# Kernel optimization log

Measured on AMD Instinct MI355X. Metric: run time of the kernel, lower is better.

## Reference

```python
import jax, jax.numpy as jnp
import numpy as np

T, B, D, NQ = 2048, 256, 128, 4  # time, batch, input_dim, n_qubits(=hidden_dim)
H = NQ


def setup_inputs() -> dict:
    key = jax.random.key(0)
    ks = jax.random.split(key, 13)
    inp = {"inputs": jax.random.normal(ks[0], (T, B, D), dtype=jnp.float32)}
    s = 1.0 / np.sqrt(D + H)  # nn.Linear default init bound
    for idx, name in enumerate(["forget", "input", "update", "output"]):
        kw, kb, kt = jax.random.split(ks[1 + idx], 3)
        inp[f"W_{name}"] = jax.random.uniform(kw, (D + H, NQ), jnp.float32, -s, s)
        inp[f"b_{name}"] = jax.random.uniform(kb, (NQ,), jnp.float32, -s, s)
        # trainable RX angles of the quantum gate layer
        inp[f"theta_{name}"] = jax.random.uniform(kt, (NQ,), jnp.float32, 0.0, 2.0 * np.pi)
    return inp


def _qlayer(x, theta):
    """Analytic simulation of the QLayer circuit.

    Circuit: RX(x_i) then RX(theta_i) on wire i (== RX(x_i+theta_i) on |0>),
    then CNOT chain (0->1, 1->2, ...), then <Z_k> on every wire.
    Heisenberg picture: Z_k pulled back through the CNOT chain becomes
    Z_0 Z_1 ... Z_k, and on the product state <Z_i> = cos(x_i + theta_i),
    so the measurement on wire k is the cumulative product of cosines.
    """
    return jnp.cumprod(jnp.cos(x + theta), axis=-1)


def reference(inputs, W_forget, b_forget, theta_forget,
              W_input, b_input, theta_input,
              W_update, b_update, theta_update,
              W_output, b_output, theta_output):
    bsz = inputs.shape[1]
    hd = theta_forget.shape[0]  # hidden_dim == n_qubits
    h0 = jnp.zeros((bsz, hd), inputs.dtype)
    c0 = jnp.zeros((bsz, hd), inputs.dtype)

    def step(carry, x):
        hx, cx = carry
        comb = jnp.concatenate([x, hx], axis=1)          # [B, D+H]
        f = jax.nn.sigmoid(_qlayer(comb @ W_forget + b_forget, theta_forget))
        i = jax.nn.sigmoid(_qlayer(comb @ W_input + b_input, theta_input))
        g = jnp.tanh(_qlayer(comb @ W_update + b_update, theta_update))
        o = jax.nn.sigmoid(_qlayer(comb @ W_output + b_output, theta_output))
        cx = f * cx + i * g
        hx = o * jnp.tanh(cx)
        return (hx, cx), hx

    (hx, cx), outputs = jax.lax.scan(step, (h0, c0), inputs)
    return outputs, hx, cx
```

## Files before the change

kernel.cpp:

```cpp
#include <hip/hip_runtime.h>
#include <hip/hip_bf16.h>

#define T_STEPS 2048
#define BATCH   256
#define DIM     128
#define INV2PI  0.15915494309189535f

#define ZX_FLOATS (T_STEPS * BATCH * 16)

__global__ __launch_bounds__(64) void prep(
    const float* __restrict__ Wf, const float* __restrict__ bf, const float* __restrict__ tf,
    const float* __restrict__ Wi, const float* __restrict__ bi, const float* __restrict__ ti,
    const float* __restrict__ Wu, const float* __restrict__ bu, const float* __restrict__ tu,
    const float* __restrict__ Wo, const float* __restrict__ bo, const float* __restrict__ to_,
    float* __restrict__ Wc, float* __restrict__ bt)
{
    const int tid = threadIdx.x;
    for (int idx = tid; idx < DIM * 16; idx += 64) {
        int d = idx >> 4, u = idx & 15, g = u >> 2, k = u & 3;
        const float* W = (g == 0) ? Wf : (g == 1) ? Wi : (g == 2) ? Wu : Wo;
        Wc[idx] = W[d * 4 + k] * INV2PI;
    }
    if (tid < 16) {
        int g = tid >> 2, k = tid & 3;
        const float* bb = (g == 0) ? bf : (g == 1) ? bi : (g == 2) ? bo : bo;
        const float* tt = (g == 0) ? tf : (g == 1) ? ti : (g == 2) ? tu : to_;
        const float* btab[4] = { bf, bi, bu, bo };
        const float* ttab[4] = { tf, ti, tu, to_ };
        bb = btab[g]; tt = ttab[g];
        bt[tid] = (bb[k] + tt[k]) * INV2PI;
    }
}

__global__ __launch_bounds__(256) void zx_gemm(
    const float4* __restrict__ x4,
    const float*  __restrict__ Wc,
    const float*  __restrict__ btv,
    float4*       __restrict__ Zx4)
{
    __shared__ float xs[4][64 * 36];
    const int lane = threadIdx.x & 63;
    const int wid  = threadIdx.x >> 6;
    float* myxs = xs[wid];
    const size_t wrow0 = ((size_t)blockIdx.x * 4 + wid) * 64;

    float acc[16];
#pragma unroll
    for (int u = 0; u < 16; ++u) acc[u] = btv[u];

    const int r0 = lane >> 3;
    const int q  = lane & 7;

#pragma unroll
    for (int c = 0; c < 4; ++c) {
        float4 v[8];
#pragma unroll
        for (int i = 0; i < 8; ++i)
            v[i] = x4[(wrow0 + i * 8 + r0) * 32 + c * 8 + q];
#pragma unroll
        for (int i = 0; i < 8; ++i)
            *(float4*)&myxs[(i * 8 + r0) * 36 + q * 4] = v[i];

        float xr[32];
#pragma unroll
        for (int j = 0; j < 8; ++j) {
            float4 tv = *(const float4*)&myxs[lane * 36 + j * 4];
            xr[j * 4 + 0] = tv.x; xr[j * 4 + 1] = tv.y;
            xr[j * 4 + 2] = tv.z; xr[j * 4 + 3] = tv.w;
        }
#pragma unroll
        for (int dd = 0; dd < 32; ++dd) {
            const float xv = xr[dd];
            const float* w = &Wc[(c * 32 + dd) * 16];
#pragma unroll
            for (int u = 0; u < 16; ++u) acc[u] = fmaf(xv, w[u], acc[u]);
        }
    }

    size_t orow = wrow0 + lane;
    float4* zr = &Zx4[orow * 4];
    zr[0] = make_float4(acc[0],  acc[1],  acc[2],  acc[3]);
    zr[1] = make_float4(acc[4],  acc[5],  acc[6],  acc[7]);
    zr[2] = make_float4(acc[8],  acc[9],  acc[10], acc[11]);
    zr[3] = make_float4(acc[12], acc[13], acc[14], acc[15]);
}

template<int CTRL>
__device__ __forceinline__ float fdpp(float x) {
    return __int_as_float(__builtin_amdgcn_update_dpp(
        0, __float_as_int(x), CTRL, 0xF, 0xF, true));
}

__device__ __forceinline__ float lstm_step(
    float& h, float& c, float zb,
    float wh0, float wh1, float wh2, float wh3,
    float s1c, float m2, float m3, int k, bool b0g, bool b1g)
{
    float h0 = fdpp<0x00>(h), h1 = fdpp<0x55>(h), h2 = fdpp<0xAA>(h), h3 = fdpp<0xFF>(h);
    float t1 = fmaf(h2, wh2, h3 * wh3);
    float z  = fmaf(h1, wh1, fmaf(h0, wh0, zb)) + t1;

    float cs = __builtin_amdgcn_cosf(__builtin_amdgcn_fractf(z));

    float q0 = fdpp<0x00>(cs), q1 = fdpp<0x55>(cs), q2 = fdpp<0xAA>(cs);
    float p = (q0 * (k >= 1 ? q1 : 1.f)) * ((k >= 2 ? q2 : 1.f) * (k == 3 ? cs : 1.f));

    float e = __builtin_amdgcn_exp2f(p * s1c);
    float y = fmaf(__builtin_amdgcn_rcpf(1.f + e), m2, m3);

    float mm  = fdpp<0x1B>(y);
    float y4  = fdpp<0x141>(mm);
    float y8  = fdpp<0x128>(y);
    float y12 = fdpp<0x128>(y4);
    float t01  = b0g ? y4  : y,  t01s = b0g ? y  : y4;
    float t23  = b0g ? y12 : y8, t23s = b0g ? y8 : y12;
    float fv = b1g ? t23  : t01;
    float iv = b1g ? t23s : t01s;
    float gv = b1g ? t01  : t23;
    float ov = b1g ? t01s : t23s;

    c = fmaf(fv, c, iv * gv);
    float e2 = __builtin_amdgcn_exp2f(c * -2.885390082f);
    float th = fmaf(2.f, __builtin_amdgcn_rcpf(1.f + e2), -1.f);
    h = ov * th;
    return h;
}

__global__ __launch_bounds__(64) void qlstm_rec(
    const float* __restrict__ Zx,
    const float* __restrict__ Wf, const float* __restrict__ Wi,
    const float* __restrict__ Wu, const float* __restrict__ Wo,
    float* __restrict__ out)
{
    const int tid = threadIdx.x;
    const int u   = tid & 15;
    const int g   = u >> 2;
    const int k   = u & 3;
    const int b   = blockIdx.x * 4 + (tid >> 4);

    const float* Wg = (g == 0) ? Wf : (g == 1) ? Wi : (g == 2) ? Wu : Wo;
    const float wh0 = Wg[(DIM + 0) * 4 + k] * INV2PI;
    const float wh1 = Wg[(DIM + 1) * 4 + k] * INV2PI;
    const float wh2 = Wg[(DIM + 2) * 4 + k] * INV2PI;
    const float wh3 = Wg[(DIM + 3) * 4 + k] * INV2PI;

    const bool  isg = (g == 2);
    const float s1c = isg ? -2.885390082f : -1.442695041f;
    const float m2  = isg ? 2.f : 1.f;
    const float m3  = isg ? -1.f : 0.f;
    const bool  b0g = (g & 1) != 0;
    const bool  b1g = (g & 2) != 0;

    const float* zp = Zx + b * 16 + u;
    const bool do_store = (u < 4);
    float* op = out + b * 4 + k;

    float h = 0.f, c = 0.f;

    float zv[8];
#pragma unroll
    for (int i = 0; i < 8; ++i) zv[i] = zp[(size_t)i * 4096];

    for (int t = 0; t < T_STEPS; t += 8) {
#pragma unroll
        for (int j = 0; j < 8; ++j) {
            int tt = t + j;

            float o = lstm_step(h, c, zv[j], wh0, wh1, wh2, wh3, s1c, m2, m3, k, b0g, b1g);

            if (do_store) op[(size_t)tt * (BATCH * 4)] = o;

            int tn = tt + 8;
            if (tn > T_STEPS - 1) tn = T_STEPS - 1;
            zv[j] = zp[(size_t)tn * 4096];
        }
    }

    if (do_store) {
        size_t hx_off = (size_t)T_STEPS * BATCH * 4;
        out[hx_off + b * 4 + k] = h;
        out[hx_off + BATCH * 4 + b * 4 + k] = c;
    }
}

extern "C" void kernel_launch(void* const* d_in, const int* in_sizes, int n_in,
                              void* d_out, int out_size, void* d_ws, size_t ws_size,
                              hipStream_t stream) {
    const float* x  = (const float*)d_in[0];
    const float* Wf = (const float*)d_in[1];
    const float* bf = (const float*)d_in[2];
    const float* tf = (const float*)d_in[3];
    const float* Wi = (const float*)d_in[4];
    const float* bi = (const float*)d_in[5];
    const float* ti = (const float*)d_in[6];
    const float* Wu = (const float*)d_in[7];
    const float* bu = (const float*)d_in[8];
    const float* tu = (const float*)d_in[9];
    const float* Wo = (const float*)d_in[10];
    const float* bo = (const float*)d_in[11];
    const float* to_ = (const float*)d_in[12];
    float* out = (float*)d_out;

    float* Zx = (float*)d_ws;
    float* Wc = Zx + ZX_FLOATS;
    float* bt = Wc + DIM * 16;

    prep<<<1, 64, 0, stream>>>(Wf, bf, tf, Wi, bi, ti, Wu, bu, tu, Wo, bo, to_, Wc, bt);

    zx_gemm<<<(T_STEPS * BATCH) / 256, 256, 0, stream>>>(
        (const float4*)x, Wc, bt, (float4*)Zx);

    qlstm_rec<<<BATCH / 4, 64, 0, stream>>>(Zx, Wf, Wi, Wu, Wo, out);
}
```

Before: 676.7 us.

## Fuse input projection GEMM into recurrent LSTM kernel with double-buffered LDS staging

```diff
diff --git a/kernel.cpp b/kernel.cpp
--- a/kernel.cpp
+++ b/kernel.cpp
@@ -5,8 +5,6 @@
 #define BATCH   256
 #define DIM     128
 #define INV2PI  0.15915494309189535f
-
-#define ZX_FLOATS (T_STEPS * BATCH * 16)
 
 __global__ __launch_bounds__(64) void prep(
     const float* __restrict__ Wf, const float* __restrict__ bf, const float* __restrict__ tf,
@@ -23,66 +21,10 @@
     }
     if (tid < 16) {
         int g = tid >> 2, k = tid & 3;
-        const float* bb = (g == 0) ? bf : (g == 1) ? bi : (g == 2) ? bo : bo;
+        const float* bb = (g == 0) ? bf : (g == 1) ? bi : (g == 2) ? bu : bo;
         const float* tt = (g == 0) ? tf : (g == 1) ? ti : (g == 2) ? tu : to_;
-        const float* btab[4] = { bf, bi, bu, bo };
-        const float* ttab[4] = { tf, ti, tu, to_ };
-        bb = btab[g]; tt = ttab[g];
         bt[tid] = (bb[k] + tt[k]) * INV2PI;
     }
-}
-
-__global__ __launch_bounds__(256) void zx_gemm(
-    const float4* __restrict__ x4,
-    const float*  __restrict__ Wc,
-    const float*  __restrict__ btv,
-    float4*       __restrict__ Zx4)
-{
-    __shared__ float xs[4][64 * 36];
-    const int lane = threadIdx.x & 63;
-    const int wid  = threadIdx.x >> 6;
-    float* myxs = xs[wid];
-    const size_t wrow0 = ((size_t)blockIdx.x * 4 + wid) * 64;
-
-    float acc[16];
-#pragma unroll
-    for (int u = 0; u < 16; ++u) acc[u] = btv[u];
-
-    const int r0 = lane >> 3;
-    const int q  = lane & 7;
-
-#pragma unroll
-    for (int c = 0; c < 4; ++c) {
-        float4 v[8];
-#pragma unroll
-        for (int i = 0; i < 8; ++i)
-            v[i] = x4[(wrow0 + i * 8 + r0) * 32 + c * 8 + q];
-#pragma unroll
-        for (int i = 0; i < 8; ++i)
-            *(float4*)&myxs[(i * 8 + r0) * 36 + q * 4] = v[i];
-
-        float xr[32];
-#pragma unroll
-        for (int j = 0; j < 8; ++j) {
-            float4 tv = *(const float4*)&myxs[lane * 36 + j * 4];
-            xr[j * 4 + 0] = tv.x; xr[j * 4 + 1] = tv.y;
-            xr[j * 4 + 2] = tv.z; xr[j * 4 + 3] = tv.w;
-        }
-#pragma unroll
-        for (int dd = 0; dd < 32; ++dd) {
-            const float xv = xr[dd];
-            const float* w = &Wc[(c * 32 + dd) * 16];
-#pragma unroll
-            for (int u = 0; u < 16; ++u) acc[u] = fmaf(xv, w[u], acc[u]);
-        }
-    }
-
-    size_t orow = wrow0 + lane;
-    float4* zr = &Zx4[orow * 4];
-    zr[0] = make_float4(acc[0],  acc[1],  acc[2],  acc[3]);
-    zr[1] = make_float4(acc[4],  acc[5],  acc[6],  acc[7]);
-    zr[2] = make_float4(acc[8],  acc[9],  acc[10], acc[11]);
-    zr[3] = make_float4(acc[12], acc[13], acc[14], acc[15]);
 }
 
 template<int CTRL>
@@ -126,17 +68,27 @@
     return h;
 }
 
-__global__ __launch_bounds__(64) void qlstm_rec(
-    const float* __restrict__ Zx,
+__global__ __launch_bounds__(64) void qlstm_fused(
+    const float4* __restrict__ x4,
+    const float*  __restrict__ Wc,
+    const float*  __restrict__ btv,
     const float* __restrict__ Wf, const float* __restrict__ Wi,
     const float* __restrict__ Wu, const float* __restrict__ Wo,
     float* __restrict__ out)
 {
+    __shared__ float xbuf[2][32 * 144];
+
     const int tid = threadIdx.x;
+    const int q   = tid >> 4;
     const int u   = tid & 15;
     const int g   = u >> 2;
     const int k   = u & 3;
-    const int b   = blockIdx.x * 4 + (tid >> 4);
+    const int b   = blockIdx.x;
+
+    float wq[32];
+#pragma unroll
+    for (int dd = 0; dd < 32; ++dd) wq[dd] = Wc[(q * 32 + dd) * 16 + u];
+    const float btu = btv[u];
 
     const float* Wg = (g == 0) ? Wf : (g == 1) ? Wi : (g == 2) ? Wu : Wo;
     const float wh0 = Wg[(DIM + 0) * 4 + k] * INV2PI;
@@ -151,29 +103,79 @@
     const bool  b0g = (g & 1) != 0;
     const bool  b1g = (g & 2) != 0;
 
-    const float* zp = Zx + b * 16 + u;
-    const bool do_store = (u < 4);
+    const bool do_store = (tid < 4);
     float* op = out + b * 4 + k;
 
     float h = 0.f, c = 0.f;
-
-    float zv[8];
-#pragma unroll
-    for (int i = 0; i < 8; ++i) zv[i] = zp[(size_t)i * 4096];
-
-    for (int t = 0; t < T_STEPS; t += 8) {
-#pragma unroll
-        for (int j = 0; j < 8; ++j) {
-            int tt = t + j;
-
-            float o = lstm_step(h, c, zv[j], wh0, wh1, wh2, wh3, s1c, m2, m3, k, b0g, b1g);
-
-            if (do_store) op[(size_t)tt * (BATCH * 4)] = o;
-
-            int tn = tt + 8;
-            if (tn > T_STEPS - 1) tn = T_STEPS - 1;
-            zv[j] = zp[(size_t)tn * 4096];
-        }
+    int pb = 0;
+
+    float4 sx[16];
+
+    auto stage_load = [&](int w) {
+        const int t0 = w * 32;
+#pragma unroll
+        for (int m = 0; m < 16; ++m) {
+            int G = m * 64 + tid, s = G >> 5, cc = G & 31;
+            sx[m] = x4[((size_t)(t0 + s) * BATCH + b) * 32 + cc];
+        }
+    };
+    auto stage_write = [&](int dst) {
+#pragma unroll
+        for (int m = 0; m < 16; ++m) {
+            int G = m * 64 + tid, s = G >> 5, cc = G & 31;
+            *(float4*)&xbuf[dst][s * 144 + (cc >> 3) * 36 + (cc & 7) * 4] = sx[m];
+        }
+    };
+    auto zx_full = [&](int slot, int buf) -> float {
+        const float* xp = &xbuf[buf][slot * 144 + q * 36];
+        float a0 = 0.f, a1 = 0.f;
+#pragma unroll
+        for (int j = 0; j < 8; j += 2) {
+            float4 xa = *(const float4*)&xp[j * 4];
+            float4 xb = *(const float4*)&xp[j * 4 + 4];
+            a0 = fmaf(xa.x, wq[4 * j + 0], a0);
+            a0 = fmaf(xa.y, wq[4 * j + 1], a0);
+            a0 = fmaf(xa.z, wq[4 * j + 2], a0);
+            a0 = fmaf(xa.w, wq[4 * j + 3], a0);
+            a1 = fmaf(xb.x, wq[4 * j + 4], a1);
+            a1 = fmaf(xb.y, wq[4 * j + 5], a1);
+            a1 = fmaf(xb.z, wq[4 * j + 6], a1);
+            a1 = fmaf(xb.w, wq[4 * j + 7], a1);
+        }
+        float v = a0 + a1;
+        v += __shfl_xor(v, 32);
+        v += __shfl_xor(v, 16);
+        return v + btu;
+    };
+
+    stage_load(0);
+    stage_write(0);
+    float zxc = zx_full(0, 0);
+
+    for (int w = 0; w < 64; ++w) {
+        if (w < 63) stage_load(w + 1);
+#pragma unroll 4
+        for (int s = 0; s < 16; ++s) {
+            float zxn = zx_full(s + 1, pb);
+            float o = lstm_step(h, c, zxc, wh0, wh1, wh2, wh3, s1c, m2, m3, k, b0g, b1g);
+            if (do_store) op[(size_t)(w * 32 + s) * (BATCH * 4)] = o;
+            zxc = zxn;
+        }
+        if (w < 63) stage_write(pb ^ 1);
+#pragma unroll 3
+        for (int s = 16; s < 31; ++s) {
+            float zxn = zx_full(s + 1, pb);
+            float o = lstm_step(h, c, zxc, wh0, wh1, wh2, wh3, s1c, m2, m3, k, b0g, b1g);
+            if (do_store) op[(size_t)(w * 32 + s) * (BATCH * 4)] = o;
+            zxc = zxn;
+        }
+        {
+            float zxn = zx_full(0, pb ^ 1);
+            float o = lstm_step(h, c, zxc, wh0, wh1, wh2, wh3, s1c, m2, m3, k, b0g, b1g);
+            if (do_store) op[(size_t)(w * 32 + 31) * (BATCH * 4)] = o;
+            zxc = zxn;
+        }
+        pb ^= 1;
     }
 
     if (do_store) {
@@ -201,14 +203,11 @@
     const float* to_ = (const float*)d_in[12];
     float* out = (float*)d_out;
 
-    float* Zx = (float*)d_ws;
-    float* Wc = Zx + ZX_FLOATS;
+    float* Wc = (float*)d_ws;
     float* bt = Wc + DIM * 16;
 
     prep<<<1, 64, 0, stream>>>(Wf, bf, tf, Wi, bi, ti, Wu, bu, tu, Wo, bo, to_, Wc, bt);
 
-    zx_gemm<<<(T_STEPS * BATCH) / 256, 256, 0, stream>>>(
-        (const float4*)x, Wc, bt, (float4*)Zx);
-
-    qlstm_rec<<<BATCH / 4, 64, 0, stream>>>(Zx, Wf, Wi, Wu, Wo, out);
-}
+    qlstm_fused<<<BATCH, 64, 0, stream>>>(
+        (const float4*)x, Wc, bt, Wf, Wi, Wu, Wo, out);
+}
```

After: 937.2 us. 38.5% more time.

## Restructure input projection GEMM with register-resident weights and pipelined staging

Applied to the files above, without the earlier changes.

```diff
diff --git a/kernel.cpp b/kernel.cpp
--- a/kernel.cpp
+++ b/kernel.cpp
@@ -23,11 +23,8 @@
     }
     if (tid < 16) {
         int g = tid >> 2, k = tid & 3;
-        const float* bb = (g == 0) ? bf : (g == 1) ? bi : (g == 2) ? bo : bo;
+        const float* bb = (g == 0) ? bf : (g == 1) ? bi : (g == 2) ? bu : bo;
         const float* tt = (g == 0) ? tf : (g == 1) ? ti : (g == 2) ? tu : to_;
-        const float* btab[4] = { bf, bi, bu, bo };
-        const float* ttab[4] = { tf, ti, tu, to_ };
-        bb = btab[g]; tt = ttab[g];
         bt[tid] = (bb[k] + tt[k]) * INV2PI;
     }
 }
@@ -36,53 +33,79 @@
     const float4* __restrict__ x4,
     const float*  __restrict__ Wc,
     const float*  __restrict__ btv,
-    float4*       __restrict__ Zx4)
-{
-    __shared__ float xs[4][64 * 36];
+    float*        __restrict__ Zx)
+{
+    __shared__ float xs[4][16 * 144];
     const int lane = threadIdx.x & 63;
     const int wid  = threadIdx.x >> 6;
     float* myxs = xs[wid];
-    const size_t wrow0 = ((size_t)blockIdx.x * 4 + wid) * 64;
-
-    float acc[16];
-#pragma unroll
-    for (int u = 0; u < 16; ++u) acc[u] = btv[u];
-
-    const int r0 = lane >> 3;
-    const int q  = lane & 7;
-
-#pragma unroll
-    for (int c = 0; c < 4; ++c) {
-        float4 v[8];
-#pragma unroll
-        for (int i = 0; i < 8; ++i)
-            v[i] = x4[(wrow0 + i * 8 + r0) * 32 + c * 8 + q];
-#pragma unroll
-        for (int i = 0; i < 8; ++i)
-            *(float4*)&myxs[(i * 8 + r0) * 36 + q * 4] = v[i];
-
-        float xr[32];
-#pragma unroll
-        for (int j = 0; j < 8; ++j) {
-            float4 tv = *(const float4*)&myxs[lane * 36 + j * 4];
-            xr[j * 4 + 0] = tv.x; xr[j * 4 + 1] = tv.y;
-            xr[j * 4 + 2] = tv.z; xr[j * 4 + 3] = tv.w;
-        }
-#pragma unroll
-        for (int dd = 0; dd < 32; ++dd) {
-            const float xv = xr[dd];
-            const float* w = &Wc[(c * 32 + dd) * 16];
-#pragma unroll
-            for (int u = 0; u < 16; ++u) acc[u] = fmaf(xv, w[u], acc[u]);
-        }
-    }
-
-    size_t orow = wrow0 + lane;
-    float4* zr = &Zx4[orow * 4];
-    zr[0] = make_float4(acc[0],  acc[1],  acc[2],  acc[3]);
-    zr[1] = make_float4(acc[4],  acc[5],  acc[6],  acc[7]);
-    zr[2] = make_float4(acc[8],  acc[9],  acc[10], acc[11]);
-    zr[3] = make_float4(acc[12], acc[13], acc[14], acc[15]);
+
+    const int q = lane >> 4;
+    const int u = lane & 15;
+
+    float wq[32];
+#pragma unroll
+    for (int dd = 0; dd < 32; ++dd) wq[dd] = Wc[(q * 32 + dd) * 16 + u];
+    const float btu = btv[u];
+
+    const size_t WR0 = ((size_t)blockIdx.x * 4 + wid) * 128;
+
+    float4 sx[8];
+    auto stage_load = [&](size_t r0) {
+#pragma unroll
+        for (int m = 0; m < 8; ++m) {
+            int G = m * 64 + lane, s = G >> 5, cc = G & 31;
+            sx[m] = x4[(r0 + s) * 32 + cc];
+        }
+    };
+    auto stage_write = [&]() {
+#pragma unroll
+        for (int m = 0; m < 8; ++m) {
+            int G = m * 64 + lane, s = G >> 5, cc = G & 31;
+            *(float4*)&myxs[s * 144 + (cc >> 3) * 36 + (cc & 7) * 4] = sx[m];
+        }
+    };
+    auto zx_row = [&](int r) -> float {
+        const float* xp = &myxs[r * 144 + q * 36];
+        float a0 = 0.f, a1 = 0.f;
+#pragma unroll
+        for (int j = 0; j < 8; j += 2) {
+            float4 xa = *(const float4*)&xp[j * 4];
+            float4 xb = *(const float4*)&xp[j * 4 + 4];
+            a0 = fmaf(xa.x, wq[4 * j + 0], a0);
+            a0 = fmaf(xa.y, wq[4 * j + 1], a0);
+            a0 = fmaf(xa.z, wq[4 * j + 2], a0);
+            a0 = fmaf(xa.w, wq[4 * j + 3], a0);
+            a1 = fmaf(xb.x, wq[4 * j + 4], a1);
+            a1 = fmaf(xb.y, wq[4 * j + 5], a1);
+            a1 = fmaf(xb.z, wq[4 * j + 6], a1);
+            a1 = fmaf(xb.w, wq[4 * j + 7], a1);
+        }
+        float v = a0 + a1;
+        v += __shfl_xor(v, 32);
+        v += __shfl_xor(v, 16);
+        return v + btu;
+    };
+
+    stage_load(WR0);
+    stage_write();
+
+    for (int i = 0; i < 8; ++i) {
+        const size_t r0 = WR0 + (size_t)i * 16;
+        if (i < 7) stage_load(r0 + 16);
+
+#pragma unroll
+        for (int rr = 0; rr < 16; rr += 4) {
+            float z0 = zx_row(rr + 0);
+            float z1 = zx_row(rr + 1);
+            float z2 = zx_row(rr + 2);
+            float z3 = zx_row(rr + 3);
+            float vout = (q == 0) ? z0 : (q == 1) ? z1 : (q == 2) ? z2 : z3;
+            Zx[(r0 + rr + q) * 16 + u] = vout;
+        }
+
+        if (i < 7) stage_write();
+    }
 }
 
 template<int CTRL>
@@ -207,8 +230,8 @@
 
     prep<<<1, 64, 0, stream>>>(Wf, bf, tf, Wi, bi, ti, Wu, bu, tu, Wo, bo, to_, Wc, bt);
 
-    zx_gemm<<<(T_STEPS * BATCH) / 256, 256, 0, stream>>>(
-        (const float4*)x, Wc, bt, (float4*)Zx);
+    zx_gemm<<<(T_STEPS * BATCH) / 512, 256, 0, stream>>>(
+        (const float4*)x, Wc, bt, Zx);
 
     qlstm_rec<<<BATCH / 4, 64, 0, stream>>>(Zx, Wf, Wi, Wu, Wo, out);
 }
```

Result: slower. 721.7 us (+6.7%).

## Merge input GEMM and recurrence into one kernel with windowed flag sync

Applied to the files above, without the earlier changes.

```diff
diff --git a/kernel.cpp b/kernel.cpp
--- a/kernel.cpp
+++ b/kernel.cpp
@@ -7,13 +7,17 @@
 #define INV2PI  0.15915494309189535f
 
 #define ZX_FLOATS (T_STEPS * BATCH * 16)
+#define NTILES   8192
+#define NWIN     64
+#define TPW      128
+#define NGEMMW   960
 
 __global__ __launch_bounds__(64) void prep(
     const float* __restrict__ Wf, const float* __restrict__ bf, const float* __restrict__ tf,
     const float* __restrict__ Wi, const float* __restrict__ bi, const float* __restrict__ ti,
     const float* __restrict__ Wu, const float* __restrict__ bu, const float* __restrict__ tu,
     const float* __restrict__ Wo, const float* __restrict__ bo, const float* __restrict__ to_,
-    float* __restrict__ Wc, float* __restrict__ bt)
+    float* __restrict__ Wc, float* __restrict__ bt, unsigned int* __restrict__ wcnt)
 {
     const int tid = threadIdx.x;
     for (int idx = tid; idx < DIM * 16; idx += 64) {
@@ -23,66 +27,11 @@
     }
     if (tid < 16) {
         int g = tid >> 2, k = tid & 3;
-        const float* bb = (g == 0) ? bf : (g == 1) ? bi : (g == 2) ? bo : bo;
+        const float* bb = (g == 0) ? bf : (g == 1) ? bi : (g == 2) ? bu : bo;
         const float* tt = (g == 0) ? tf : (g == 1) ? ti : (g == 2) ? tu : to_;
-        const float* btab[4] = { bf, bi, bu, bo };
-        const float* ttab[4] = { tf, ti, tu, to_ };
-        bb = btab[g]; tt = ttab[g];
         bt[tid] = (bb[k] + tt[k]) * INV2PI;
     }
-}
-
-__global__ __launch_bounds__(256) void zx_gemm(
-    const float4* __restrict__ x4,
-    const float*  __restrict__ Wc,
-    const float*  __restrict__ btv,
-    float4*       __restrict__ Zx4)
-{
-    __shared__ float xs[4][64 * 36];
-    const int lane = threadIdx.x & 63;
-    const int wid  = threadIdx.x >> 6;
-    float* myxs = xs[wid];
-    const size_t wrow0 = ((size_t)blockIdx.x * 4 + wid) * 64;
-
-    float acc[16];
-#pragma unroll
-    for (int u = 0; u < 16; ++u) acc[u] = btv[u];
-
-    const int r0 = lane >> 3;
-    const int q  = lane & 7;
-
-#pragma unroll
-    for (int c = 0; c < 4; ++c) {
-        float4 v[8];
-#pragma unroll
-        for (int i = 0; i < 8; ++i)
-            v[i] = x4[(wrow0 + i * 8 + r0) * 32 + c * 8 + q];
-#pragma unroll
-        for (int i = 0; i < 8; ++i)
-            *(float4*)&myxs[(i * 8 + r0) * 36 + q * 4] = v[i];
-
-        float xr[32];
-#pragma unroll
-        for (int j = 0; j < 8; ++j) {
-            float4 tv = *(const float4*)&myxs[lane * 36 + j * 4];
-            xr[j * 4 + 0] = tv.x; xr[j * 4 + 1] = tv.y;
-            xr[j * 4 + 2] = tv.z; xr[j * 4 + 3] = tv.w;
-        }
-#pragma unroll
-        for (int dd = 0; dd < 32; ++dd) {
-            const float xv = xr[dd];
-            const float* w = &Wc[(c * 32 + dd) * 16];
-#pragma unroll
-            for (int u = 0; u < 16; ++u) acc[u] = fmaf(xv, w[u], acc[u]);
-        }
-    }
-
-    size_t orow = wrow0 + lane;
-    float4* zr = &Zx4[orow * 4];
-    zr[0] = make_float4(acc[0],  acc[1],  acc[2],  acc[3]);
-    zr[1] = make_float4(acc[4],  acc[5],  acc[6],  acc[7]);
-    zr[2] = make_float4(acc[8],  acc[9],  acc[10], acc[11]);
-    zr[3] = make_float4(acc[12], acc[13], acc[14], acc[15]);
+    __hip_atomic_store(&wcnt[tid], 0u, __ATOMIC_RELAXED, __HIP_MEMORY_SCOPE_AGENT);
 }
 
 template<int CTRL>
@@ -126,60 +75,148 @@
     return h;
 }
 
-__global__ __launch_bounds__(64) void qlstm_rec(
-    const float* __restrict__ Zx,
+__device__ __forceinline__ void wave_poll(unsigned int* wcnt, int w, int lane) {
+    for (;;) {
+        unsigned v = 0;
+        if (lane == 0)
+            v = __hip_atomic_fetch_add(&wcnt[w], 0u, __ATOMIC_ACQUIRE,
+                                       __HIP_MEMORY_SCOPE_AGENT);
+        v = (unsigned)__builtin_amdgcn_readfirstlane((int)v);
+        if (v >= (unsigned)TPW) break;
+        __builtin_amdgcn_s_sleep(4);
+    }
+    __builtin_amdgcn_fence(__ATOMIC_ACQUIRE, "agent");
+}
+
+__global__ __launch_bounds__(256) void qlstm_merged(
+    const float4* __restrict__ x4,
+    const float*  __restrict__ Wc,
+    const float*  __restrict__ btv,
     const float* __restrict__ Wf, const float* __restrict__ Wi,
     const float* __restrict__ Wu, const float* __restrict__ Wo,
+    float* __restrict__ Zx,
+    unsigned int* __restrict__ wcnt,
     float* __restrict__ out)
 {
-    const int tid = threadIdx.x;
-    const int u   = tid & 15;
-    const int g   = u >> 2;
-    const int k   = u & 3;
-    const int b   = blockIdx.x * 4 + (tid >> 4);
-
-    const float* Wg = (g == 0) ? Wf : (g == 1) ? Wi : (g == 2) ? Wu : Wo;
-    const float wh0 = Wg[(DIM + 0) * 4 + k] * INV2PI;
-    const float wh1 = Wg[(DIM + 1) * 4 + k] * INV2PI;
-    const float wh2 = Wg[(DIM + 2) * 4 + k] * INV2PI;
-    const float wh3 = Wg[(DIM + 3) * 4 + k] * INV2PI;
-
-    const bool  isg = (g == 2);
-    const float s1c = isg ? -2.885390082f : -1.442695041f;
-    const float m2  = isg ? 2.f : 1.f;
-    const float m3  = isg ? -1.f : 0.f;
-    const bool  b0g = (g & 1) != 0;
-    const bool  b1g = (g & 2) != 0;
-
-    const float* zp = Zx + b * 16 + u;
-    const bool do_store = (u < 4);
-    float* op = out + b * 4 + k;
-
-    float h = 0.f, c = 0.f;
-
-    float zv[8];
-#pragma unroll
-    for (int i = 0; i < 8; ++i) zv[i] = zp[(size_t)i * 4096];
-
-    for (int t = 0; t < T_STEPS; t += 8) {
-#pragma unroll
-        for (int j = 0; j < 8; ++j) {
-            int tt = t + j;
-
-            float o = lstm_step(h, c, zv[j], wh0, wh1, wh2, wh3, s1c, m2, m3, k, b0g, b1g);
-
-            if (do_store) op[(size_t)tt * (BATCH * 4)] = o;
-
-            int tn = tt + 8;
-            if (tn > T_STEPS - 1) tn = T_STEPS - 1;
-            zv[j] = zp[(size_t)tn * 4096];
+    __shared__ float xs[4][64 * 36];
+    const int bi   = blockIdx.x;
+    const int wi   = threadIdx.x >> 6;
+    const int lane = threadIdx.x & 63;
+    const bool is_rec = (bi >= 192) && (wi == 3);
+
+    if (!is_rec) {
+        float* myxs = xs[wi];
+        const int rank = (bi < 192) ? (bi * 4 + wi) : (768 + (bi - 192) * 3 + wi);
+        const int r0 = lane >> 3;
+        const int q  = lane & 7;
+
+        float acc0[16];
+#pragma unroll
+        for (int u = 0; u < 16; ++u) acc0[u] = btv[u];
+
+        float4* Zx4 = (float4*)Zx;
+
+        for (int tile = rank; tile < NTILES; tile += NGEMMW) {
+            const size_t wrow0 = (size_t)tile * 64;
+            float acc[16];
+#pragma unroll
+            for (int u = 0; u < 16; ++u) acc[u] = acc0[u];
+
+#pragma unroll
+            for (int c = 0; c < 4; ++c) {
+                float4 v[8];
+#pragma unroll
+                for (int i = 0; i < 8; ++i)
+                    v[i] = x4[(wrow0 + i * 8 + r0) * 32 + c * 8 + q];
+#pragma unroll
+                for (int i = 0; i < 8; ++i)
+                    *(float4*)&myxs[(i * 8 + r0) * 36 + q * 4] = v[i];
+
+                float xr[32];
+#pragma unroll
+                for (int j = 0; j < 8; ++j) {
+                    float4 tv = *(const float4*)&myxs[lane * 36 + j * 4];
+                    xr[j * 4 + 0] = tv.x; xr[j * 4 + 1] = tv.y;
+                    xr[j * 4 + 2] = tv.z; xr[j * 4 + 3] = tv.w;
+                }
+#pragma unroll
+                for (int dd = 0; dd < 32; ++dd) {
+                    const float xv = xr[dd];
+                    const float* w = &Wc[(c * 32 + dd) * 16];
+#pragma unroll
+                    for (int u = 0; u < 16; ++u) acc[u] = fmaf(xv, w[u], acc[u]);
+                }
+            }
+
+            size_t orow = wrow0 + lane;
+            float4* zr = &Zx4[orow * 4];
+            zr[0] = make_float4(acc[0],  acc[1],  acc[2],  acc[3]);
+            zr[1] = make_float4(acc[4],  acc[5],  acc[6],  acc[7]);
+            zr[2] = make_float4(acc[8],  acc[9],  acc[10], acc[11]);
+            zr[3] = make_float4(acc[12], acc[13], acc[14], acc[15]);
+
+            __builtin_amdgcn_fence(__ATOMIC_RELEASE, "agent");
+            if (lane == 0)
+                __hip_atomic_fetch_add(&wcnt[tile >> 7], 1u,
+                                       __ATOMIC_RELEASE, __HIP_MEMORY_SCOPE_AGENT);
         }
-    }
-
-    if (do_store) {
-        size_t hx_off = (size_t)T_STEPS * BATCH * 4;
-        out[hx_off + b * 4 + k] = h;
-        out[hx_off + BATCH * 4 + b * 4 + k] = c;
+    } else {
+        __builtin_amdgcn_s_setprio(2);
+
+        const int u = lane & 15;
+        const int g = u >> 2;
+        const int k = u & 3;
+        const int b = (bi - 192) * 4 + (lane >> 4);
+
+        const float* Wg = (g == 0) ? Wf : (g == 1) ? Wi : (g == 2) ? Wu : Wo;
+        const float wh0 = Wg[(DIM + 0) * 4 + k] * INV2PI;
+        const float wh1 = Wg[(DIM + 1) * 4 + k] * INV2PI;
+        const float wh2 = Wg[(DIM + 2) * 4 + k] * INV2PI;
+        const float wh3 = Wg[(DIM + 3) * 4 + k] * INV2PI;
+
+        const bool  isg = (g == 2);
+        const float s1c = isg ? -2.885390082f : -1.442695041f;
+        const float m2  = isg ? 2.f : 1.f;
+        const float m3  = isg ? -1.f : 0.f;
+        const bool  b0g = (g & 1) != 0;
+        const bool  b1g = (g & 2) != 0;
+
+        const float* zp = Zx + b * 16 + u;
+        const bool do_store = (u < 4);
+        float* op = out + b * 4 + k;
+
+        float h = 0.f, c = 0.f;
+
+        wave_poll(wcnt, 0, lane);
+
+        float zv[8];
+#pragma unroll
+        for (int i = 0; i < 8; ++i) zv[i] = zp[(size_t)i * 4096];
+
+        int wcur = 0;
+        for (int t = 0; t < T_STEPS; t += 8) {
+            int wneed = (t + 15) >> 5;
+            if (wneed > wcur && wneed < NWIN) { wave_poll(wcnt, wneed, lane); wcur = wneed; }
+
+#pragma unroll
+            for (int j = 0; j < 8; ++j) {
+                int tt = t + j;
+
+                float o = lstm_step(h, c, zv[j], wh0, wh1, wh2, wh3, s1c, m2, m3, k, b0g, b1g);
+
+                if (do_store) op[(size_t)tt * (BATCH * 4)] = o;
+
+                int tn = tt + 8;
+                if (tn > T_STEPS - 1) tn = T_STEPS - 1;
+                zv[j] = zp[(size_t)tn * 4096];
+            }
+        }
+
+        if (do_store) {
+            size_t hx_off = (size_t)T_STEPS * BATCH * 4;
+            out[hx_off + b * 4 + k] = h;
+            out[hx_off + BATCH * 4 + b * 4 + k] = c;
+        }
     }
 }
 
@@ -204,11 +241,11 @@
     float* Zx = (float*)d_ws;
     float* Wc = Zx + ZX_FLOATS;
     float* bt = Wc + DIM * 16;
-
-    prep<<<1, 64, 0, stream>>>(Wf, bf, tf, Wi, bi, ti, Wu, bu, tu, Wo, bo, to_, Wc, bt);
-
-    zx_gemm<<<(T_STEPS * BATCH) / 256, 256, 0, stream>>>(
-        (const float4*)x, Wc, bt, (float4*)Zx);
-
-    qlstm_rec<<<BATCH / 4, 64, 0, stream>>>(Zx, Wf, Wi, Wu, Wo, out);
-}
+    unsigned int* wcnt = (unsigned int*)(bt + 16);
+
+    prep<<<1, 64, 0, stream>>>(Wf, bf, tf, Wi, bi, ti, Wu, bu, tu, Wo, bo, to_,
+                               Wc, bt, wcnt);
+
+    qlstm_merged<<<256, 256, 0, stream>>>(
+        (const float4*)x, Wc, bt, Wf, Wi, Wu, Wo, Zx, wcnt, out);
+}
```

Measured after the change: 1.310 ms. 93.6% more time.
